# Kernel optimization log

Measured on AMD Instinct MI355X. Metric: run time of the kernel, lower is better.

The kernel has to match this reference:

```python
import jax, jax.numpy as jnp
import numpy as np

NUM_HEADS = 16
HEAD_DIM = 128  # 2048 / 16


def setup_inputs() -> dict:
    key = jax.random.key(0)
    ks = jax.random.split(key, 5)
    B, S, D = 2, 2048, 2048
    scale = 1.0 / np.sqrt(D)
    return {
        "x": jax.random.normal(ks[0], (B, S, D), dtype=jnp.float32),
        "Wq": jax.random.normal(ks[1], (D, D), dtype=jnp.float32) * scale,
        "Wk": jax.random.normal(ks[2], (D, D), dtype=jnp.float32) * scale,
        "Wv": jax.random.normal(ks[3], (D, D), dtype=jnp.float32) * scale,
        "Wo": jax.random.normal(ks[4], (D, D), dtype=jnp.float32) * scale,
    }


def reference(x, Wq, Wk, Wv, Wo):
    B, S, D = x.shape
    H, Hd = NUM_HEADS, HEAD_DIM
    # nn.Linear(bias=False): y = x @ W.T
    q = (x @ Wq.T).reshape(B, S, H, Hd).transpose(0, 2, 1, 3)  # [B,H,S,Hd]
    k = (x @ Wk.T).reshape(B, S, H, Hd).transpose(0, 2, 1, 3)
    v = (x @ Wv.T).reshape(B, S, H, Hd).transpose(0, 2, 1, 3)
    scores = jnp.einsum("bhqd,bhkd->bhqk", q, k) / jnp.sqrt(jnp.float32(Hd))
    attn = jax.nn.softmax(scores, axis=-1)  # dropout p=0 (eval) -> identity
    out = jnp.einsum("bhqk,bhkd->bhqd", attn, v)  # [B,H,S,Hd]
    out = out.transpose(0, 2, 1, 3).reshape(B, S, D)
    out = out @ Wo.T
    return out
```

## Files before the change

### kernel.cpp

```cpp
#include <hip/hip_runtime.h>
#include <math.h>
#include <stdint.h>


#define DDIM 2048
#define SEQ  2048
#define NH   16
#define HD   128

typedef __attribute__((ext_vector_type(4))) float f32x4;
typedef __attribute__((ext_vector_type(16))) float f32x16;
typedef __attribute__((ext_vector_type(8))) __bf16 bf16x8;
typedef __attribute__((ext_vector_type(4))) unsigned int u32x4;
typedef __attribute__((ext_vector_type(2))) unsigned int u32x2;

#define MFMA_B16(a, b, c) __builtin_amdgcn_mfma_f32_16x16x32_bf16((a), (b), (c), 0, 0, 0)
#define MFMA32(a, b, c) __builtin_amdgcn_mfma_f32_32x32x16_bf16((a), (b), (c), 0, 0, 0)

__device__ __forceinline__ void async16(const void* g, void* l) {
  __builtin_amdgcn_global_load_lds(
      (const __attribute__((address_space(1))) unsigned int*)g,
      (__attribute__((address_space(3))) unsigned int*)l, 16, 0, 0);
}

__device__ __forceinline__ unsigned short f2bf(float f) {
  unsigned u = __builtin_bit_cast(unsigned, f);
  u += 0x7fffu + ((u >> 16) & 1u);
  return (unsigned short)(u >> 16);
}

__device__ __forceinline__ bf16x8 ldfrag(const unsigned short* p) {
  return __builtin_bit_cast(bf16x8, *(const u32x4*)p);
}

__device__ __forceinline__ void cvt_body(const float* __restrict__ s,
                                         unsigned short* __restrict__ d, int i) {
  const f32x4* sp = (const f32x4*)s;
  f32x4 a = sp[2 * i], b = sp[2 * i + 1];
  u32x4 o;
  o.x = ((unsigned)f2bf(a.y) << 16) | f2bf(a.x);
  o.y = ((unsigned)f2bf(a.w) << 16) | f2bf(a.z);
  o.z = ((unsigned)f2bf(b.y) << 16) | f2bf(b.x);
  o.w = ((unsigned)f2bf(b.w) << 16) | f2bf(b.z);
  ((u32x4*)d)[i] = o;
}

__global__ __launch_bounds__(256) void cvt_bf16_kernel(const float* __restrict__ s,
                                                       unsigned short* __restrict__ d) {
  cvt_body(s, d, blockIdx.x * 256 + threadIdx.x);
}

__global__ __launch_bounds__(256) void cvt_all_kernel(const float* __restrict__ x,
                                                      const float* __restrict__ wq,
                                                      const float* __restrict__ wk,
                                                      const float* __restrict__ wv,
                                                      const float* __restrict__ wo,
                                                      unsigned short* __restrict__ xb,
                                                      unsigned short* __restrict__ wqkv,
                                                      unsigned short* __restrict__ wob) {
  const int b = blockIdx.x;
  if (b < 4096) {
    cvt_body(x, xb, b * 256 + threadIdx.x);
  } else if (b < 10240) {
    const int wi = (b - 4096) >> 11, lb = (b - 4096) & 2047;
    const float* s = (wi == 0) ? wq : (wi == 1) ? wk : wv;
    cvt_body(s, wqkv + (size_t)wi * 4194304u, lb * 256 + threadIdx.x);
  } else {
    cvt_body(wo, wob, (b - 10240) * 256 + threadIdx.x);
  }
}

__global__ __launch_bounds__(256) void gemm_qkv(const unsigned short* __restrict__ A,
                                                const unsigned short* __restrict__ B,
                                                unsigned short* __restrict__ Oqk,
                                                unsigned short* __restrict__ Ovt,
                                                float alpha_q) {
  __shared__ unsigned short As[128 * 64];
  __shared__ unsigned short Bs[128 * 64];
  const int tid = threadIdx.x;
  const int lane = tid & 63, w = tid >> 6;
  const int l32 = lane & 31, half = lane >> 5;
  const int wm = (w >> 1) * 64, wn = (w & 1) * 64;
  const int bm = blockIdx.y * 128, bn = blockIdx.x * 128;

  f32x16 acc[2][2];
#pragma unroll
  for (int i = 0; i < 2; ++i)
#pragma unroll
    for (int j = 0; j < 2; ++j)
#pragma unroll
      for (int e = 0; e < 16; ++e) acc[i][j][e] = 0.f;

  const unsigned short* pa[4];
  const unsigned short* pbb[4];
  {
#pragma unroll
    for (int j = 0; j < 4; ++j) {
      const int row = j * 32 + (tid >> 3);
      const int cg = (tid & 7) ^ (row & 7) ^ ((row >> 3) & 7);
      pa[j] = A + (size_t)(bm + row) * DDIM + cg * 8;
      pbb[j] = B + (size_t)(bn + row) * DDIM + cg * 8;
    }
  }

  const int fr = (l32 & 7) ^ (l32 >> 3);

  for (int kt = 0; kt < 32; ++kt) {
    __syncthreads();
#pragma unroll
    for (int j = 0; j < 4; ++j) {
      async16(pa[j], &As[(j * 256 + tid) * 8]);
      pa[j] += 64;
      async16(pbb[j], &Bs[(j * 256 + tid) * 8]);
      pbb[j] += 64;
    }
    __syncthreads();
#pragma unroll
    for (int ks = 0; ks < 4; ++ks) {
      const int ph = ks * 2 + half;
      const int sl0 = (ph ^ fr) * 8;
      const int sl1 = (ph ^ fr ^ 4) * 8;
      bf16x8 af0 = ldfrag(&As[(wm + l32) * 64 + sl0]);
      bf16x8 af1 = ldfrag(&As[(wm + 32 + l32) * 64 + sl1]);
      bf16x8 bf0 = ldfrag(&Bs[(wn + l32) * 64 + sl0]);
      bf16x8 bf1 = ldfrag(&Bs[(wn + 32 + l32) * 64 + sl1]);
      acc[0][0] = MFMA32(af0, bf0, acc[0][0]);
      acc[0][1] = MFMA32(af0, bf1, acc[0][1]);
      acc[1][0] = MFMA32(af1, bf0, acc[1][0]);
      acc[1][1] = MFMA32(af1, bf1, acc[1][1]);
    }
  }

  const int seg = bn >> 11;
  const int bnl = bn & 2047;
  const float alpha = (seg == 0) ? alpha_q : 1.0f;
#pragma unroll
  for (int i = 0; i < 2; ++i) {
#pragma unroll
    for (int j = 0; j < 2; ++j) {
#pragma unroll
      for (int rg = 0; rg < 4; ++rg) {
        const int m0 = bm + wm + i * 32 + rg * 8 + half * 4;
        const float v0 = acc[i][j][rg * 4 + 0] * alpha;
        const float v1 = acc[i][j][rg * 4 + 1] * alpha;
        const float v2 = acc[i][j][rg * 4 + 2] * alpha;
        const float v3 = acc[i][j][rg * 4 + 3] * alpha;
        const int n = bnl + wn + j * 32 + l32;
        if (seg < 2) {
          unsigned short* O = Oqk + (size_t)seg * (4096u * 2048u);
          O[(size_t)(m0 + 0) * DDIM + n] = f2bf(v0);
          O[(size_t)(m0 + 1) * DDIM + n] = f2bf(v1);
          O[(size_t)(m0 + 2) * DDIM + n] = f2bf(v2);
          O[(size_t)(m0 + 3) * DDIM + n] = f2bf(v3);
        } else {
          const int bb = m0 >> 11, s0 = m0 & 2047;
          const int hh = n >> 7, dd = n & 127;
          u32x2 st;
          st.x = ((unsigned)f2bf(v1) << 16) | f2bf(v0);
          st.y = ((unsigned)f2bf(v3) << 16) | f2bf(v2);
          *(u32x2*)&Ovt[((size_t)((bb * NH + hh) * HD + dd)) * SEQ + s0] = st;
        }
      }
    }
  }
}

__global__ __launch_bounds__(256) void gemm_o64(const unsigned short* __restrict__ A,
                                                const unsigned short* __restrict__ B,
                                                float* __restrict__ Cf) {
  __shared__ unsigned short As[128 * 64];
  __shared__ unsigned short Bs[64 * 64];
  const int tid = threadIdx.x;
  const int lane = tid & 63, w = tid >> 6;
  const int l32 = lane & 31, half = lane >> 5;
  const int wm = (w >> 1) * 64, wn = (w & 1) * 32;
  const int bm = blockIdx.y * 128, bn = blockIdx.x * 64;

  f32x16 acc[2];
#pragma unroll
  for (int i = 0; i < 2; ++i)
#pragma unroll
    for (int e = 0; e < 16; ++e) acc[i][e] = 0.f;

  const unsigned short* pa[4];
  const unsigned short* pbb[2];
  {
#pragma unroll
    for (int j = 0; j < 4; ++j) {
      const int row = j * 32 + (tid >> 3);
      const int cg = (tid & 7) ^ (row & 7) ^ ((row >> 3) & 7);
      pa[j] = A + (size_t)(bm + row) * DDIM + cg * 8;
      if (j < 2) pbb[j] = B + (size_t)(bn + row) * DDIM + cg * 8;
    }
  }

  const int fr = (l32 & 7) ^ (l32 >> 3);
  const int fb = fr ^ ((wn >> 3) & 4);

  for (int kt = 0; kt < 32; ++kt) {
    __syncthreads();
#pragma unroll
    for (int j = 0; j < 4; ++j) {
      async16(pa[j], &As[(j * 256 + tid) * 8]);
      pa[j] += 64;
      if (j < 2) {
        async16(pbb[j], &Bs[(j * 256 + tid) * 8]);
        pbb[j] += 64;
      }
    }
    __syncthreads();
#pragma unroll
    for (int ks = 0; ks < 4; ++ks) {
      const int ph = ks * 2 + half;
      bf16x8 af0 = ldfrag(&As[(wm + l32) * 64 + (ph ^ fr) * 8]);
      bf16x8 af1 = ldfrag(&As[(wm + 32 + l32) * 64 + (ph ^ fr ^ 4) * 8]);
      bf16x8 bf0 = ldfrag(&Bs[(wn + l32) * 64 + (ph ^ fb) * 8]);
      acc[0] = MFMA32(af0, bf0, acc[0]);
      acc[1] = MFMA32(af1, bf0, acc[1]);
    }
  }

#pragma unroll
  for (int i = 0; i < 2; ++i) {
#pragma unroll
    for (int rg = 0; rg < 4; ++rg) {
      const int m0 = bm + wm + i * 32 + rg * 8 + half * 4;
      const int n = bn + wn + l32;
      Cf[(size_t)(m0 + 0) * DDIM + n] = acc[i][rg * 4 + 0];
      Cf[(size_t)(m0 + 1) * DDIM + n] = acc[i][rg * 4 + 1];
      Cf[(size_t)(m0 + 2) * DDIM + n] = acc[i][rg * 4 + 2];
      Cf[(size_t)(m0 + 3) * DDIM + n] = acc[i][rg * 4 + 3];
    }
  }
}

__global__ __launch_bounds__(512) void attn_kernel(const unsigned short* __restrict__ qb,
                                                   const unsigned short* __restrict__ kb,
                                                   const unsigned short* __restrict__ vtb,
                                                   unsigned short* __restrict__ ab) {
  __shared__ unsigned short Ks[64 * 128];
  __shared__ unsigned short Vts[128 * 64];
  __shared__ unsigned short Pw[8 * 16 * 40];
  const int tid = threadIdx.x;
  const int w = tid >> 6, lane = tid & 63;
  const int quad = lane >> 4, l16 = lane & 15;
  const int qt = blockIdx.x, bh = blockIdx.y;
  const int b = bh >> 4, h = bh & 15;
  const int qrow = qt * 128 + w * 16 + l16;

  const unsigned short* qp = qb + ((size_t)(b * SEQ + qrow)) * DDIM + h * HD;
  bf16x8 qf[4];
#pragma unroll
  for (int ks = 0; ks < 4; ++ks) qf[ks] = ldfrag(qp + ks * 32 + quad * 8);

  f32x4 ot[8];
#pragma unroll
  for (int i = 0; i < 8; i++) ot[i] = f32x4{0.f, 0.f, 0.f, 0.f};
  float sumacc = 0.f;

  const unsigned short* kp[2];
  const unsigned short* vp[2];
  {
    const size_t kbase = ((size_t)(b * SEQ)) * DDIM + h * HD;
    const size_t vbase = ((size_t)((b * NH + h) * HD)) * SEQ;
#pragma unroll
    for (int j = 0; j < 2; ++j) {
      const int key = j * 32 + (tid >> 4), cgk = (tid & 15) ^ (key & 15);
      kp[j] = kb + kbase + (size_t)key * DDIM + cgk * 8;
      const int dd = j * 64 + (tid >> 3), cgv = (tid & 7) ^ (dd & 7);
      vp[j] = vtb + vbase + (size_t)dd * SEQ + cgv * 8;
    }
  }
  unsigned short* pw = &Pw[w * 640];

  for (int kt = 0; kt < SEQ / 64; ++kt) {
    __syncthreads();
#pragma unroll
    for (int j = 0; j < 2; ++j) {
      async16(kp[j], &Ks[(j * 512 + tid) * 8]);
      kp[j] += (size_t)64 * DDIM;
      async16(vp[j], &Vts[(j * 512 + tid) * 8]);
      vp[j] += 64;
    }
    __syncthreads();
    f32x4 s[4];
#pragma unroll
    for (int t = 0; t < 4; ++t) s[t] = f32x4{0.f, 0.f, 0.f, 0.f};
#pragma unroll
    for (int ks = 0; ks < 4; ++ks) {
      const int sl = ((ks * 4 + quad) ^ l16) * 8;
#pragma unroll
      for (int t = 0; t < 4; ++t) {
        bf16x8 a = ldfrag(&Ks[(t * 16 + l16) * 128 + sl]);
        s[t] = MFMA_B16(a, qf[ks], s[t]);
      }
    }
    f32x4 p[4];
#pragma unroll
    for (int t = 0; t < 4; ++t) {
      p[t].x = __builtin_amdgcn_exp2f(s[t].x);
      p[t].y = __builtin_amdgcn_exp2f(s[t].y);
      p[t].z = __builtin_amdgcn_exp2f(s[t].z);
      p[t].w = __builtin_amdgcn_exp2f(s[t].w);
      sumacc += (p[t].x + p[t].y) + (p[t].z + p[t].w);
    }
    bf16x8 pb0, pb1;
    {
      u32x2 w0, w1;
      w0.x = ((unsigned)f2bf(p[0].y) << 16) | f2bf(p[0].x);
      w0.y = ((unsigned)f2bf(p[0].w) << 16) | f2bf(p[0].z);
      w1.x = ((unsigned)f2bf(p[1].y) << 16) | f2bf(p[1].x);
      w1.y = ((unsigned)f2bf(p[1].w) << 16) | f2bf(p[1].z);
      *(u32x2*)&pw[l16 * 40 + quad * 4] = w0;
      *(u32x2*)&pw[l16 * 40 + 16 + quad * 4] = w1;
      asm volatile("s_waitcnt lgkmcnt(0)" ::: "memory");
      pb0 = ldfrag(&pw[l16 * 40 + quad * 8]);
      w0.x = ((unsigned)f2bf(p[2].y) << 16) | f2bf(p[2].x);
      w0.y = ((unsigned)f2bf(p[2].w) << 16) | f2bf(p[2].z);
      w1.x = ((unsigned)f2bf(p[3].y) << 16) | f2bf(p[3].x);
      w1.y = ((unsigned)f2bf(p[3].w) << 16) | f2bf(p[3].z);
      *(u32x2*)&pw[l16 * 40 + quad * 4] = w0;
      *(u32x2*)&pw[l16 * 40 + 16 + quad * 4] = w1;
      asm volatile("s_waitcnt lgkmcnt(0)" ::: "memory");
      pb1 = ldfrag(&pw[l16 * 40 + quad * 8]);
    }
#pragma unroll
    for (int mt = 0; mt < 8; ++mt) {
      bf16x8 vf0 = ldfrag(&Vts[(mt * 16 + l16) * 64 + (quad ^ (l16 & 7)) * 8]);
      ot[mt] = MFMA_B16(vf0, pb0, ot[mt]);
      bf16x8 vf1 = ldfrag(&Vts[(mt * 16 + l16) * 64 + ((4 + quad) ^ (l16 & 7)) * 8]);
      ot[mt] = MFMA_B16(vf1, pb1, ot[mt]);
    }
  }
  float total = sumacc;
  total += __shfl_xor(total, 16);
  total += __shfl_xor(total, 32);
  const float inv = 1.0f / total;
  unsigned short* op = ab + ((size_t)(b * SEQ + qrow)) * DDIM + h * HD;
#pragma unroll
  for (int mt = 0; mt < 8; ++mt) {
    f32x4 v = ot[mt] * inv;
    u32x2 st;
    st.x = ((unsigned)f2bf(v.y) << 16) | f2bf(v.x);
    st.y = ((unsigned)f2bf(v.w) << 16) | f2bf(v.z);
    *(u32x2*)&op[mt * 16 + quad * 4] = st;
  }
}

extern "C" void kernel_launch(void* const* d_in, const int* in_sizes, int n_in,
                              void* d_out, int out_size, void* d_ws, size_t ws_size,
                              hipStream_t stream) {
  (void)in_sizes; (void)n_in; (void)out_size;
  const float* x = (const float*)d_in[0];
  const float* Wq = (const float*)d_in[1];
  const float* Wk = (const float*)d_in[2];
  const float* Wv = (const float*)d_in[3];
  const float* Wo = (const float*)d_in[4];

  char* ws = (char*)d_ws;
  unsigned short* xb = (unsigned short*)(ws);
  unsigned short* wqkv = (unsigned short*)(ws + 16777216);
  unsigned short* qb = (unsigned short*)(ws + 41943040);
  unsigned short* kb = (unsigned short*)(ws + 58720256);
  unsigned short* vtb = (unsigned short*)(ws + 75497472);
  const bool big = ws_size >= 100663296ull;
  unsigned short* wob = big ? (unsigned short*)(ws + 92274688) : wqkv;

  const float alpha_q = 1.44269504088896341f / sqrtf(128.0f);

  if (big) {
    cvt_all_kernel<<<dim3(12288), 256, 0, stream>>>(x, Wq, Wk, Wv, Wo, xb, wqkv, wob);
    gemm_qkv<<<dim3(48, 32), 256, 0, stream>>>(xb, wqkv, qb, vtb, alpha_q);
  } else {
    cvt_all_kernel<<<dim3(10240), 256, 0, stream>>>(x, Wq, Wk, Wv, Wo, xb, wqkv, wob);
    gemm_qkv<<<dim3(48, 32), 256, 0, stream>>>(xb, wqkv, qb, vtb, alpha_q);
    cvt_bf16_kernel<<<dim3(2048), 256, 0, stream>>>(Wo, wob);
  }

  attn_kernel<<<dim3(16, 32), 512, 0, stream>>>(qb, kb, vtb, xb);

  gemm_o64<<<dim3(32, 32), 256, 0, stream>>>(xb, wob, (float*)d_out);
}
```

Measured before the change: 366.2 us.

## Switch attention kernel to 32x32 MFMA tiles with 4 waves of 32 query rows

The attention kernel moves from 16x16x32 MFMA with 8 waves of 16 query rows to 32x32x16 MFMA with 4 waves of 32 query rows per block. The goal is to raise arithmetic intensity per LDS fragment load and cut the number of P round-trips through shared memory, since the whole 32x64 P tile is written once and then read back. The K and V shared-memory swizzles are redone for the new access pattern. The price is more accumulator registers per lane and half as many waves per block, which may lower occupancy and latency hiding.

Result: slower. 397.9 us (+8.6%).

```diff
diff --git a/kernel.cpp b/kernel.cpp
--- a/kernel.cpp
+++ b/kernel.cpp
@@ -234,116 +234,115 @@
   }
 }
 
-__global__ __launch_bounds__(512) void attn_kernel(const unsigned short* __restrict__ qb,
+__global__ __launch_bounds__(256) void attn_kernel(const unsigned short* __restrict__ qb,
                                                    const unsigned short* __restrict__ kb,
                                                    const unsigned short* __restrict__ vtb,
                                                    unsigned short* __restrict__ ab) {
   __shared__ unsigned short Ks[64 * 128];
   __shared__ unsigned short Vts[128 * 64];
-  __shared__ unsigned short Pw[8 * 16 * 40];
+  __shared__ unsigned short Pw[4 * 32 * 68];
   const int tid = threadIdx.x;
   const int w = tid >> 6, lane = tid & 63;
-  const int quad = lane >> 4, l16 = lane & 15;
+  const int l32 = lane & 31, half = lane >> 5;
   const int qt = blockIdx.x, bh = blockIdx.y;
   const int b = bh >> 4, h = bh & 15;
-  const int qrow = qt * 128 + w * 16 + l16;
+  const int qrow = qt * 128 + w * 32 + l32;
 
   const unsigned short* qp = qb + ((size_t)(b * SEQ + qrow)) * DDIM + h * HD;
-  bf16x8 qf[4];
-#pragma unroll
-  for (int ks = 0; ks < 4; ++ks) qf[ks] = ldfrag(qp + ks * 32 + quad * 8);
-
-  f32x4 ot[8];
-#pragma unroll
-  for (int i = 0; i < 8; i++) ot[i] = f32x4{0.f, 0.f, 0.f, 0.f};
+  bf16x8 qf[8];
+#pragma unroll
+  for (int st = 0; st < 8; ++st) qf[st] = ldfrag(qp + st * 16 + half * 8);
+
+  f32x16 ot[4];
+#pragma unroll
+  for (int i = 0; i < 4; ++i)
+#pragma unroll
+    for (int e = 0; e < 16; ++e) ot[i][e] = 0.f;
   float sumacc = 0.f;
 
-  const unsigned short* kp[2];
-  const unsigned short* vp[2];
+  const unsigned short* kp[4];
+  const unsigned short* vp[4];
   {
     const size_t kbase = ((size_t)(b * SEQ)) * DDIM + h * HD;
     const size_t vbase = ((size_t)((b * NH + h) * HD)) * SEQ;
 #pragma unroll
-    for (int j = 0; j < 2; ++j) {
-      const int key = j * 32 + (tid >> 4), cgk = (tid & 15) ^ (key & 15);
+    for (int j = 0; j < 4; ++j) {
+      const int key = j * 16 + (tid >> 4);
+      const int cgk = (tid & 15) ^ (tid >> 4);
       kp[j] = kb + kbase + (size_t)key * DDIM + cgk * 8;
-      const int dd = j * 64 + (tid >> 3), cgv = (tid & 7) ^ (dd & 7);
+      const int dd = j * 32 + (tid >> 3);
+      const int cgv = (tid & 7) ^ (dd & 7) ^ ((dd >> 3) & 7);
       vp[j] = vtb + vbase + (size_t)dd * SEQ + cgv * 8;
     }
   }
-  unsigned short* pw = &Pw[w * 640];
+  unsigned short* pw = &Pw[w * (32 * 68)];
+  int fv[4];
+#pragma unroll
+  for (int dt = 0; dt < 4; ++dt) fv[dt] = (l32 & 7) ^ ((dt * 4 + (l32 >> 3)) & 7);
 
   for (int kt = 0; kt < SEQ / 64; ++kt) {
     __syncthreads();
 #pragma unroll
-    for (int j = 0; j < 2; ++j) {
-      async16(kp[j], &Ks[(j * 512 + tid) * 8]);
+    for (int j = 0; j < 4; ++j) {
+      async16(kp[j], &Ks[(j * 256 + tid) * 8]);
       kp[j] += (size_t)64 * DDIM;
-      async16(vp[j], &Vts[(j * 512 + tid) * 8]);
+      async16(vp[j], &Vts[(j * 256 + tid) * 8]);
       vp[j] += 64;
     }
     __syncthreads();
-    f32x4 s[4];
-#pragma unroll
-    for (int t = 0; t < 4; ++t) s[t] = f32x4{0.f, 0.f, 0.f, 0.f};
-#pragma unroll
-    for (int ks = 0; ks < 4; ++ks) {
-      const int sl = ((ks * 4 + quad) ^ l16) * 8;
-#pragma unroll
-      for (int t = 0; t < 4; ++t) {
-        bf16x8 a = ldfrag(&Ks[(t * 16 + l16) * 128 + sl]);
-        s[t] = MFMA_B16(a, qf[ks], s[t]);
-      }
-    }
-    f32x4 p[4];
-#pragma unroll
-    for (int t = 0; t < 4; ++t) {
-      p[t].x = __builtin_amdgcn_exp2f(s[t].x);
-      p[t].y = __builtin_amdgcn_exp2f(s[t].y);
-      p[t].z = __builtin_amdgcn_exp2f(s[t].z);
-      p[t].w = __builtin_amdgcn_exp2f(s[t].w);
-      sumacc += (p[t].x + p[t].y) + (p[t].z + p[t].w);
-    }
-    bf16x8 pb0, pb1;
-    {
-      u32x2 w0, w1;
-      w0.x = ((unsigned)f2bf(p[0].y) << 16) | f2bf(p[0].x);
-      w0.y = ((unsigned)f2bf(p[0].w) << 16) | f2bf(p[0].z);
-      w1.x = ((unsigned)f2bf(p[1].y) << 16) | f2bf(p[1].x);
-      w1.y = ((unsigned)f2bf(p[1].w) << 16) | f2bf(p[1].z);
-      *(u32x2*)&pw[l16 * 40 + quad * 4] = w0;
-      *(u32x2*)&pw[l16 * 40 + 16 + quad * 4] = w1;
-      asm volatile("s_waitcnt lgkmcnt(0)" ::: "memory");
-      pb0 = ldfrag(&pw[l16 * 40 + quad * 8]);
-      w0.x = ((unsigned)f2bf(p[2].y) << 16) | f2bf(p[2].x);
-      w0.y = ((unsigned)f2bf(p[2].w) << 16) | f2bf(p[2].z);
-      w1.x = ((unsigned)f2bf(p[3].y) << 16) | f2bf(p[3].x);
-      w1.y = ((unsigned)f2bf(p[3].w) << 16) | f2bf(p[3].z);
-      *(u32x2*)&pw[l16 * 40 + quad * 4] = w0;
-      *(u32x2*)&pw[l16 * 40 + 16 + quad * 4] = w1;
-      asm volatile("s_waitcnt lgkmcnt(0)" ::: "memory");
-      pb1 = ldfrag(&pw[l16 * 40 + quad * 8]);
-    }
-#pragma unroll
-    for (int mt = 0; mt < 8; ++mt) {
-      bf16x8 vf0 = ldfrag(&Vts[(mt * 16 + l16) * 64 + (quad ^ (l16 & 7)) * 8]);
-      ot[mt] = MFMA_B16(vf0, pb0, ot[mt]);
-      bf16x8 vf1 = ldfrag(&Vts[(mt * 16 + l16) * 64 + ((4 + quad) ^ (l16 & 7)) * 8]);
-      ot[mt] = MFMA_B16(vf1, pb1, ot[mt]);
-    }
-  }
-  float total = sumacc;
-  total += __shfl_xor(total, 16);
-  total += __shfl_xor(total, 32);
-  const float inv = 1.0f / total;
+    f32x16 s0, s1;
+#pragma unroll
+    for (int e = 0; e < 16; ++e) { s0[e] = 0.f; s1[e] = 0.f; }
+#pragma unroll
+    for (int st = 0; st < 8; ++st) {
+      const int sl = ((st * 2 + half) ^ (l32 & 15)) * 8;
+      bf16x8 a0 = ldfrag(&Ks[(l32) * 128 + sl]);
+      bf16x8 a1 = ldfrag(&Ks[(32 + l32) * 128 + sl]);
+      s0 = MFMA32(a0, qf[st], s0);
+      s1 = MFMA32(a1, qf[st], s1);
+    }
+#pragma unroll
+    for (int t = 0; t < 2; ++t) {
+      const f32x16& sv = t ? s1 : s0;
+      float p[16];
+#pragma unroll
+      for (int e = 0; e < 16; ++e) {
+        p[e] = __builtin_amdgcn_exp2f(sv[e]);
+        sumacc += p[e];
+      }
+#pragma unroll
+      for (int g = 0; g < 4; ++g) {
+        u32x2 pk;
+        pk.x = ((unsigned)f2bf(p[4 * g + 1]) << 16) | f2bf(p[4 * g + 0]);
+        pk.y = ((unsigned)f2bf(p[4 * g + 3]) << 16) | f2bf(p[4 * g + 2]);
+        *(u32x2*)&pw[l32 * 68 + t * 32 + g * 8 + half * 4] = pk;
+      }
+    }
+    asm volatile("s_waitcnt lgkmcnt(0)" ::: "memory");
+#pragma unroll
+    for (int kstep = 0; kstep < 4; ++kstep) {
+      bf16x8 pb = ldfrag(&pw[l32 * 68 + kstep * 16 + half * 8]);
+#pragma unroll
+      for (int dt = 0; dt < 4; ++dt) {
+        const int sl = ((kstep * 2 + half) ^ fv[dt]) * 8;
+        bf16x8 vf = ldfrag(&Vts[(dt * 32 + l32) * 64 + sl]);
+        ot[dt] = MFMA32(vf, pb, ot[dt]);
+      }
+    }
+  }
+  sumacc += __shfl_xor(sumacc, 32);
+  const float inv = 1.0f / sumacc;
   unsigned short* op = ab + ((size_t)(b * SEQ + qrow)) * DDIM + h * HD;
 #pragma unroll
-  for (int mt = 0; mt < 8; ++mt) {
-    f32x4 v = ot[mt] * inv;
-    u32x2 st;
-    st.x = ((unsigned)f2bf(v.y) << 16) | f2bf(v.x);
-    st.y = ((unsigned)f2bf(v.w) << 16) | f2bf(v.z);
-    *(u32x2*)&op[mt * 16 + quad * 4] = st;
+  for (int dt = 0; dt < 4; ++dt) {
+#pragma unroll
+    for (int g = 0; g < 4; ++g) {
+      const int d0 = dt * 32 + g * 8 + half * 4;
+      u32x2 stv;
+      stv.x = ((unsigned)f2bf(ot[dt][4 * g + 1] * inv) << 16) | f2bf(ot[dt][4 * g + 0] * inv);
+      stv.y = ((unsigned)f2bf(ot[dt][4 * g + 3] * inv) << 16) | f2bf(ot[dt][4 * g + 2] * inv);
+      *(u32x2*)&op[d0] = stv;
+    }
   }
 }
 
@@ -377,7 +376,7 @@
     cvt_bf16_kernel<<<dim3(2048), 256, 0, stream>>>(Wo, wob);
   }
 
-  attn_kernel<<<dim3(16, 32), 512, 0, stream>>>(qb, kb, vtb, xb);
+  attn_kernel<<<dim3(16, 32), 256, 0, stream>>>(qb, kb, vtb, xb);
 
   gemm_o64<<<dim3(32, 32), 256, 0, stream>>>(xb, wob, (float*)d_out);
 }
```
